# Performance work log

Measured on AMD Instinct MI355X. Metric: run time of the kernel, lower is better.

The kernel has to match this reference:

```python
import jax, jax.numpy as jnp
import numpy as np

NUM_HEADS = 32
NUM_KV_HEADS = 8  # num_heads // 4 (GQA)
HEAD_DIM = 64     # hidden_size // num_heads
ROPE_BASE = 10000.0


def _rotate_half(x):
    x1, x2 = jnp.split(x, 2, axis=-1)
    return jnp.concatenate((-x2, x1), axis=-1)


def _rope_cos_sin(seq_len, dtype):
    inv_freq = 1.0 / (ROPE_BASE ** (jnp.arange(0, HEAD_DIM, 2, dtype=jnp.float32) / HEAD_DIM))
    t = jnp.arange(seq_len, dtype=jnp.float32)
    freqs = jnp.outer(t, inv_freq)                 # [S, HEAD_DIM//2]
    emb = jnp.concatenate((freqs, freqs), axis=-1) # [S, HEAD_DIM]
    return jnp.cos(emb).astype(dtype), jnp.sin(emb).astype(dtype)


def setup_inputs() -> dict:
    key = jax.random.key(0)
    ks = jax.random.split(key, 5)
    B, S, H = 1, 2048, 2048
    KV = NUM_KV_HEADS * HEAD_DIM  # 512
    s = 0.02
    return {
        "hidden_states": jax.random.normal(ks[0], (B, S, H), jnp.float32),
        "Wq": jax.random.normal(ks[1], (H, H), jnp.float32) * s,
        "Wk": jax.random.normal(ks[2], (KV, H), jnp.float32) * s,
        "Wv": jax.random.normal(ks[3], (KV, H), jnp.float32) * s,
        "Wo": jax.random.normal(ks[4], (H, H), jnp.float32) * s,
    }


def reference(hidden_states, Wq, Wk, Wv, Wo):
    B, S, H = hidden_states.shape
    dtype = hidden_states.dtype
    # QKV projections (nn.Linear with weight [out,in], no bias)
    q = jnp.einsum("bsh,oh->bso", hidden_states, Wq)
    k = jnp.einsum("bsh,oh->bso", hidden_states, Wk)
    v = jnp.einsum("bsh,oh->bso", hidden_states, Wv)
    q = q.reshape(B, S, NUM_HEADS, HEAD_DIM).transpose(0, 2, 1, 3)      # [B,H,S,D]
    k = k.reshape(B, S, NUM_KV_HEADS, HEAD_DIM).transpose(0, 2, 1, 3)   # [B,KV,S,D]
    v = v.reshape(B, S, NUM_KV_HEADS, HEAD_DIM).transpose(0, 2, 1, 3)
    # RoPE
    cos, sin = _rope_cos_sin(S, dtype)  # [S,D] broadcast over batch/heads
    q = q * cos + _rotate_half(q) * sin
    k = k * cos + _rotate_half(k) * sin
    # GQA: repeat_interleave KV heads
    groups = NUM_HEADS // NUM_KV_HEADS
    k = jnp.repeat(k, groups, axis=1)
    v = jnp.repeat(v, groups, axis=1)
    # Attention: scores in fp32 softmax, causal mask (additive)
    scale = 1.0 / np.sqrt(HEAD_DIM)
    scores = jnp.einsum("bhqd,bhkd->bhqk", q, k) * scale
    causal = jnp.tril(jnp.ones((S, S), dtype=bool))
    scores = jnp.where(causal, scores, jnp.finfo(jnp.float32).min)
    probs = jax.nn.softmax(scores.astype(jnp.float32), axis=-1).astype(dtype)
    attn = jnp.einsum("bhqk,bhkd->bhqd", probs, v)
    attn = attn.transpose(0, 2, 1, 3).reshape(B, S, H)
    return jnp.einsum("bsh,oh->bso", attn, Wo)
```

## Files before the change

kernel.cpp:

```cpp
#include <hip/hip_runtime.h>
#include <hip/hip_bf16.h>
#include <math.h>

typedef __hip_bfloat16 bf16;
typedef __attribute__((ext_vector_type(8))) short short8;
typedef __attribute__((ext_vector_type(4))) short short4v;
typedef __attribute__((ext_vector_type(4))) float floatx4;

#define MFMA16(a, b, c) __builtin_amdgcn_mfma_f32_16x16x32_bf16((a), (b), (c), 0, 0, 0)

typedef const __attribute__((address_space(1))) void* as1_cvp;
typedef __attribute__((address_space(3))) void* as3_vp;

__device__ __forceinline__ void gload_lds16(const bf16* g, bf16* lds_uni) {
    __builtin_amdgcn_global_load_lds((as1_cvp)g, (as3_vp)lds_uni, 16, 0, 0);
}

__global__ __launch_bounds__(256) void cvt_all(
    const float* __restrict__ a0, const float* __restrict__ a1,
    const float* __restrict__ a2, const float* __restrict__ a3,
    const float* __restrict__ a4,
    bf16* __restrict__ d0, bf16* __restrict__ d1, bf16* __restrict__ d2,
    bf16* __restrict__ d3, bf16* __restrict__ d4)
{
    const int b = blockIdx.x;
    const float* src; bf16* dst; int off;
    if (b < 2048)      { src = a0; dst = d0; off = b; }
    else if (b < 4096) { src = a1; dst = d1; off = b - 2048; }
    else if (b < 4608) { src = a2; dst = d2; off = b - 4096; }
    else if (b < 5120) { src = a3; dst = d3; off = b - 4608; }
    else               { src = a4; dst = d4; off = b - 5120; }
    const int i = (off * 256 + threadIdx.x) * 8;
    const float4 x = *(const float4*)(src + i);
    const float4 y = *(const float4*)(src + i + 4);
    bf16 t[8];
    t[0] = __float2bfloat16(x.x); t[1] = __float2bfloat16(x.y);
    t[2] = __float2bfloat16(x.z); t[3] = __float2bfloat16(x.w);
    t[4] = __float2bfloat16(y.x); t[5] = __float2bfloat16(y.y);
    t[6] = __float2bfloat16(y.z); t[7] = __float2bfloat16(y.w);
    *(short8*)(dst + i) = *(const short8*)t;
}

__global__ __launch_bounds__(256) void gemm_qkv(
    const bf16* __restrict__ A, const bf16* __restrict__ Wq,
    const bf16* __restrict__ Wk, const bf16* __restrict__ Wv,
    bf16* __restrict__ qb, bf16* __restrict__ kb, bf16* __restrict__ vt)
{
    constexpr int K = 2048;
    __shared__ bf16 As[128 * 32];
    __shared__ bf16 Bs[128 * 32];

    const int tid  = threadIdx.x;
    const int lane = tid & 63;
    const int w    = tid >> 6;
    const int wm   = w >> 1, wn = w & 1;
    const int quad = lane >> 4, l15 = lane & 15;
    const int bx = blockIdx.x, by = blockIdx.y;

    const bf16* Bp; int bxl, mode;
    if (bx < 16)      { Bp = Wq; bxl = bx;      mode = 0; }
    else if (bx < 20) { Bp = Wk; bxl = bx - 16; mode = 1; }
    else              { Bp = Wv; bxl = bx - 20; mode = 2; }

    floatx4 acc[4][4];
#pragma unroll
    for (int i = 0; i < 4; ++i)
#pragma unroll
        for (int j = 0; j < 4; ++j) {
            floatx4 z = {0.f, 0.f, 0.f, 0.f};
            acc[i][j] = z;
        }

    const int srow = tid >> 2;
    const int sch  = (tid & 3) * 8;
    const bf16* gA = A  + (size_t)(by * 128 + srow) * K + sch;
    const bf16* gB = Bp + (size_t)(bxl * 128 + srow) * K + sch;
    const size_t K64 = (size_t)64 * K;
    bf16* ldsA0 = As + w * 512;
    bf16* ldsA1 = As + 2048 + w * 512;
    bf16* ldsB0 = Bs + w * 512;
    bf16* ldsB1 = Bs + 2048 + w * 512;

    for (int k0 = 0; k0 < K; k0 += 32) {
        gload_lds16(gA + k0,        ldsA0);
        gload_lds16(gA + K64 + k0,  ldsA1);
        gload_lds16(gB + k0,        ldsB0);
        gload_lds16(gB + K64 + k0,  ldsB1);
        __syncthreads();

        short8 af[4], bfrag[4];
#pragma unroll
        for (int i = 0; i < 4; ++i)
            af[i] = *(const short8*)&As[(wm * 64 + i * 16 + l15) * 32 + quad * 8];
#pragma unroll
        for (int j = 0; j < 4; ++j)
            bfrag[j] = *(const short8*)&Bs[(wn * 64 + j * 16 + l15) * 32 + quad * 8];
#pragma unroll
        for (int i = 0; i < 4; ++i)
#pragma unroll
            for (int j = 0; j < 4; ++j)
                acc[i][j] = MFMA16(af[i], bfrag[j], acc[i][j]);
        __syncthreads();
    }

    if (mode == 2) {
#pragma unroll
        for (int i = 0; i < 4; ++i)
#pragma unroll
            for (int j = 0; j < 4; ++j) {
                const int col = bxl * 128 + wn * 64 + j * 16 + l15;
                const int rowb = by * 128 + wm * 64 + i * 16 + quad * 4;
                bf16 t[4];
#pragma unroll
                for (int r = 0; r < 4; ++r) t[r] = __float2bfloat16(acc[i][j][r]);
                *(short4v*)&vt[(size_t)col * 2048 + rowb] = *(const short4v*)t;
            }
    } else {
        const int Nn = (mode == 0) ? 2048 : 512;
        bf16* C = (mode == 0) ? qb : kb;
        const float scale = (mode == 0) ? 0.125f : 1.0f;
        const float LOG2_1E4 = 13.28771237954945f;
        const float ifr0 = exp2f(-((float)l15) * (LOG2_1E4 / 32.f));
        const float ifr1 = exp2f(-((float)(16 + l15)) * (LOG2_1E4 / 32.f));
#pragma unroll
        for (int i = 0; i < 4; ++i) {
#pragma unroll
            for (int r = 0; r < 4; ++r) {
                const int row = by * 128 + wm * 64 + i * 16 + quad * 4 + r;
                float s0, c0, s1, c1;
                sincosf((float)row * ifr0, &s0, &c0);
                sincosf((float)row * ifr1, &s1, &c1);
#pragma unroll
                for (int j = 0; j < 4; ++j) {
                    const float x  = acc[i][j][r];
                    const float xp = acc[i][j ^ 2][r];
                    const float cs = (j & 1) ? c1 : c0;
                    const float sn = (j & 1) ? s1 : s0;
                    const float oo = (x * cs + ((j < 2) ? -xp : xp) * sn) * scale;
                    const int col = bxl * 128 + wn * 64 + j * 16 + l15;
                    C[(size_t)row * Nn + col] = __float2bfloat16(oo);
                }
            }
        }
    }
}

__global__ __launch_bounds__(256) void gemm_out(
    const bf16* __restrict__ A, const bf16* __restrict__ B, float* __restrict__ C,
    int N, int K)
{
    __shared__ bf16 As[128 * 32];
    __shared__ bf16 Bs[128 * 32];

    const int tid  = threadIdx.x;
    const int lane = tid & 63;
    const int w    = tid >> 6;
    const int wm   = w >> 1, wn = w & 1;
    const int quad = lane >> 4, l15 = lane & 15;
    const int bx = blockIdx.x, by = blockIdx.y;

    floatx4 acc[4][4];
#pragma unroll
    for (int i = 0; i < 4; ++i)
#pragma unroll
        for (int j = 0; j < 4; ++j) {
            floatx4 z = {0.f, 0.f, 0.f, 0.f};
            acc[i][j] = z;
        }

    const int srow = tid >> 2;
    const int sch  = (tid & 3) * 8;
    const bf16* gA = A + (size_t)(by * 128 + srow) * K + sch;
    const bf16* gB = B + (size_t)(bx * 128 + srow) * K + sch;
    const size_t K64 = (size_t)64 * K;
    bf16* ldsA0 = As + w * 512;
    bf16* ldsA1 = As + 2048 + w * 512;
    bf16* ldsB0 = Bs + w * 512;
    bf16* ldsB1 = Bs + 2048 + w * 512;

    for (int k0 = 0; k0 < K; k0 += 32) {
        gload_lds16(gA + k0,        ldsA0);
        gload_lds16(gA + K64 + k0,  ldsA1);
        gload_lds16(gB + k0,        ldsB0);
        gload_lds16(gB + K64 + k0,  ldsB1);
        __syncthreads();

        short8 af[4], bfrag[4];
#pragma unroll
        for (int i = 0; i < 4; ++i)
            af[i] = *(const short8*)&As[(wm * 64 + i * 16 + l15) * 32 + quad * 8];
#pragma unroll
        for (int j = 0; j < 4; ++j)
            bfrag[j] = *(const short8*)&Bs[(wn * 64 + j * 16 + l15) * 32 + quad * 8];
#pragma unroll
        for (int i = 0; i < 4; ++i)
#pragma unroll
            for (int j = 0; j < 4; ++j)
                acc[i][j] = MFMA16(af[i], bfrag[j], acc[i][j]);
        __syncthreads();
    }

#pragma unroll
    for (int i = 0; i < 4; ++i)
#pragma unroll
        for (int j = 0; j < 4; ++j)
#pragma unroll
            for (int r = 0; r < 4; ++r) {
                const int row = by * 128 + wm * 64 + i * 16 + quad * 4 + r;
                const int col = bx * 128 + wn * 64 + j * 16 + l15;
                C[(size_t)row * N + col] = acc[i][j][r];
            }
}

__global__ __launch_bounds__(256) void fattn4(
    const bf16* __restrict__ q, const bf16* __restrict__ k,
    const bf16* __restrict__ vt, bf16* __restrict__ o)
{
    __shared__ bf16 Ks[2][64 * 72];
    __shared__ bf16 Vs[2][64 * 72];
    __shared__ bf16 Ps[4][16 * 68];

    const int tpair = blockIdx.x;
    const int h = blockIdx.y;
    const int kvh = h >> 2;
    const int tid = threadIdx.x, lane = tid & 63, w = tid >> 6;
    const int quad = lane >> 4, l15 = lane & 15;
    bf16* P = Ps[w];

    short ob[8];
#pragma unroll
    for (int e = 0; e < 8; ++e) ob[e] = (short)0x3F80;
    const short8 ones = *(const short8*)ob;

    const int srow = tid >> 3;
    const int ch8  = (tid & 7) * 8;
    const bf16* kg = k  + (size_t)kvh * 64 + ch8;
    const bf16* vg = vt + (size_t)(kvh * 64 + srow) * 2048 + ch8;

#pragma unroll 1
    for (int ph = 0; ph < 2; ++ph) {
        const int a = ph ? (31 - tpair) : tpair;
        const int qrow0 = a * 64 + w * 16;

        short8 qf[2];
#pragma unroll
        for (int ks = 0; ks < 2; ++ks)
            qf[ks] = *(const short8*)&q[(size_t)(qrow0 + l15) * 2048 + h * 64 + ks * 32 + quad * 8];

        floatx4 o_acc[4], l_acc;
#pragma unroll
        for (int n4 = 0; n4 < 4; ++n4) {
            floatx4 z = {0.f, 0.f, 0.f, 0.f};
            o_acc[n4] = z;
        }
        { floatx4 z = {0.f, 0.f, 0.f, 0.f}; l_acc = z; }

        {
            short8 k0 = *(const short8*)(kg + (size_t)srow * 512);
            short8 k1 = *(const short8*)(kg + (size_t)(srow + 32) * 512);
            short8 v0 = *(const short8*)(vg);
            short8 v1 = *(const short8*)(vg + (size_t)32 * 2048);
            *(short8*)&Ks[0][srow * 72 + ch8]        = k0;
            *(short8*)&Ks[0][(srow + 32) * 72 + ch8] = k1;
            *(short8*)&Vs[0][srow * 72 + ch8]        = v0;
            *(short8*)&Vs[0][(srow + 32) * 72 + ch8] = v1;
        }
        __syncthreads();

        for (int kt = 0; kt <= a; ++kt) {
            const int buf = kt & 1;

            short8 nk0, nk1, nv0, nv1;
            if (kt < a) {
                const size_t kr = (size_t)((kt + 1) * 64) * 512;
                nk0 = *(const short8*)(kg + kr + (size_t)srow * 512);
                nk1 = *(const short8*)(kg + kr + (size_t)(srow + 32) * 512);
                nv0 = *(const short8*)(vg + (kt + 1) * 64);
                nv1 = *(const short8*)(vg + (size_t)32 * 2048 + (kt + 1) * 64);
            }

            floatx4 s_acc[4];
#pragma unroll
            for (int n = 0; n < 4; ++n) {
                floatx4 z = {0.f, 0.f, 0.f, 0.f};
                s_acc[n] = z;
            }
#pragma unroll
            for (int n = 0; n < 4; ++n)
#pragma unroll
                for (int ks = 0; ks < 2; ++ks) {
                    const short8 kf = *(const short8*)&Ks[buf][(n * 16 + l15) * 72 + ks * 32 + quad * 8];
                    s_acc[n] = MFMA16(qf[ks], kf, s_acc[n]);
                }

            if (kt < a) {
#pragma unroll
                for (int n = 0; n < 4; ++n)
#pragma unroll
                    for (int r = 0; r < 4; ++r)
                        P[(quad * 4 + r) * 68 + n * 16 + l15] = __float2bfloat16(__expf(s_acc[n][r]));
            } else {
#pragma unroll
                for (int n = 0; n < 4; ++n)
#pragma unroll
                    for (int r = 0; r < 4; ++r) {
                        const bool ok = (n * 16 + l15) <= (w * 16 + quad * 4 + r);
                        const float p = ok ? __expf(s_acc[n][r]) : 0.f;
                        P[(quad * 4 + r) * 68 + n * 16 + l15] = __float2bfloat16(p);
                    }
            }

#pragma unroll
            for (int ks2 = 0; ks2 < 2; ++ks2) {
                const short8 pf = *(const short8*)&P[l15 * 68 + ks2 * 32 + quad * 8];
                l_acc = MFMA16(pf, ones, l_acc);
#pragma unroll
                for (int n4 = 0; n4 < 4; ++n4) {
                    const short8 vf = *(const short8*)&Vs[buf][(n4 * 16 + l15) * 72 + ks2 * 32 + quad * 8];
                    o_acc[n4] = MFMA16(pf, vf, o_acc[n4]);
                }
            }

            if (kt < a) {
                *(short8*)&Ks[buf ^ 1][srow * 72 + ch8]        = nk0;
                *(short8*)&Ks[buf ^ 1][(srow + 32) * 72 + ch8] = nk1;
                *(short8*)&Vs[buf ^ 1][srow * 72 + ch8]        = nv0;
                *(short8*)&Vs[buf ^ 1][(srow + 32) * 72 + ch8] = nv1;
            }
            __syncthreads();
        }

#pragma unroll
        for (int n4 = 0; n4 < 4; ++n4)
#pragma unroll
            for (int r = 0; r < 4; ++r) {
                const float val = o_acc[n4][r] / l_acc[r];
                const int row = qrow0 + quad * 4 + r;
                const int col = h * 64 + n4 * 16 + l15;
                o[(size_t)row * 2048 + col] = __float2bfloat16(val);
            }
    }
}

extern "C" void kernel_launch(void* const* d_in, const int* in_sizes, int n_in,
                              void* d_out, int out_size, void* d_ws, size_t ws_size,
                              hipStream_t stream)
{
    const float* hs = (const float*)d_in[0];
    const float* Wq = (const float*)d_in[1];
    const float* Wk = (const float*)d_in[2];
    const float* Wv = (const float*)d_in[3];
    const float* Wo = (const float*)d_in[4];
    float* out = (float*)d_out;

    bf16* ws  = (bf16*)d_ws;
    bf16* hsb = ws;
    bf16* Wqb = hsb + 4194304;
    bf16* Wkb = Wqb + 4194304;
    bf16* Wvb = Wkb + 1048576;
    bf16* Wob = Wvb + 1048576;
    bf16* qb  = Wob + 4194304;
    bf16* kb  = qb  + 4194304;
    bf16* vtb = kb  + 1048576;
    bf16* ab  = vtb + 1048576;

    dim3 blk(256);
    cvt_all<<<7168, blk, 0, stream>>>(hs, Wq, Wk, Wv, Wo, hsb, Wqb, Wkb, Wvb, Wob);
    gemm_qkv<<<dim3(24, 16), blk, 0, stream>>>(hsb, Wqb, Wkb, Wvb, qb, kb, vtb);
    fattn4<<<dim3(16, 32), blk, 0, stream>>>(qb, kb, vtb, ab);
    gemm_out<<<dim3(16, 16), blk, 0, stream>>>(ab, Wob, out, 2048, 2048);
}
```

Baseline: 248.9 us.

## Double GEMM K-step and use 128-row query tiles in flash attention

```diff
diff --git a/kernel.cpp b/kernel.cpp
--- a/kernel.cpp
+++ b/kernel.cpp
@@ -41,14 +41,43 @@
     *(short8*)(dst + i) = *(const short8*)t;
 }
 
+#define GEMM_K_LOOP(K)                                                          \
+    for (int k0 = 0; k0 < (K); k0 += 64) {                                      \
+        gload_lds16(gA + k0,            ldsA0);                                 \
+        gload_lds16(gA + K64 + k0,      ldsA1);                                 \
+        gload_lds16(gB + k0,            ldsB0);                                 \
+        gload_lds16(gB + K64 + k0,      ldsB1);                                 \
+        gload_lds16(gA + k0 + 32,       ldsA0 + 4096);                          \
+        gload_lds16(gA + K64 + k0 + 32, ldsA1 + 4096);                          \
+        gload_lds16(gB + k0 + 32,       ldsB0 + 4096);                          \
+        gload_lds16(gB + K64 + k0 + 32, ldsB1 + 4096);                          \
+        __syncthreads();                                                        \
+        _Pragma("unroll")                                                       \
+        for (int hh = 0; hh < 2; ++hh) {                                        \
+            short8 af[4], bfr[4];                                               \
+            _Pragma("unroll")                                                   \
+            for (int i = 0; i < 4; ++i)                                         \
+                af[i] = *(const short8*)&As[hh * 4096 + (wm * 64 + i * 16 + l15) * 32 + quad * 8]; \
+            _Pragma("unroll")                                                   \
+            for (int j = 0; j < 4; ++j)                                         \
+                bfr[j] = *(const short8*)&Bs[hh * 4096 + (wn * 64 + j * 16 + l15) * 32 + quad * 8]; \
+            _Pragma("unroll")                                                   \
+            for (int i = 0; i < 4; ++i)                                         \
+                _Pragma("unroll")                                               \
+                for (int j = 0; j < 4; ++j)                                     \
+                    acc[i][j] = MFMA16(af[i], bfr[j], acc[i][j]);               \
+        }                                                                       \
+        __syncthreads();                                                        \
+    }
+
 __global__ __launch_bounds__(256) void gemm_qkv(
     const bf16* __restrict__ A, const bf16* __restrict__ Wq,
     const bf16* __restrict__ Wk, const bf16* __restrict__ Wv,
     bf16* __restrict__ qb, bf16* __restrict__ kb, bf16* __restrict__ vt)
 {
     constexpr int K = 2048;
-    __shared__ bf16 As[128 * 32];
-    __shared__ bf16 Bs[128 * 32];
+    __shared__ bf16 As[2 * 128 * 32];
+    __shared__ bf16 Bs[2 * 128 * 32];
 
     const int tid  = threadIdx.x;
     const int lane = tid & 63;
@@ -81,27 +110,7 @@
     bf16* ldsB0 = Bs + w * 512;
     bf16* ldsB1 = Bs + 2048 + w * 512;
 
-    for (int k0 = 0; k0 < K; k0 += 32) {
-        gload_lds16(gA + k0,        ldsA0);
-        gload_lds16(gA + K64 + k0,  ldsA1);
-        gload_lds16(gB + k0,        ldsB0);
-        gload_lds16(gB + K64 + k0,  ldsB1);
-        __syncthreads();
-
-        short8 af[4], bfrag[4];
-#pragma unroll
-        for (int i = 0; i < 4; ++i)
-            af[i] = *(const short8*)&As[(wm * 64 + i * 16 + l15) * 32 + quad * 8];
-#pragma unroll
-        for (int j = 0; j < 4; ++j)
-            bfrag[j] = *(const short8*)&Bs[(wn * 64 + j * 16 + l15) * 32 + quad * 8];
-#pragma unroll
-        for (int i = 0; i < 4; ++i)
-#pragma unroll
-            for (int j = 0; j < 4; ++j)
-                acc[i][j] = MFMA16(af[i], bfrag[j], acc[i][j]);
-        __syncthreads();
-    }
+    GEMM_K_LOOP(K)
 
     if (mode == 2) {
 #pragma unroll
@@ -149,8 +158,8 @@
     const bf16* __restrict__ A, const bf16* __restrict__ B, float* __restrict__ C,
     int N, int K)
 {
-    __shared__ bf16 As[128 * 32];
-    __shared__ bf16 Bs[128 * 32];
+    __shared__ bf16 As[2 * 128 * 32];
+    __shared__ bf16 Bs[2 * 128 * 32];
 
     const int tid  = threadIdx.x;
     const int lane = tid & 63;
@@ -178,27 +187,7 @@
     bf16* ldsB0 = Bs + w * 512;
     bf16* ldsB1 = Bs + 2048 + w * 512;
 
-    for (int k0 = 0; k0 < K; k0 += 32) {
-        gload_lds16(gA + k0,        ldsA0);
-        gload_lds16(gA + K64 + k0,  ldsA1);
-        gload_lds16(gB + k0,        ldsB0);
-        gload_lds16(gB + K64 + k0,  ldsB1);
-        __syncthreads();
-
-        short8 af[4], bfrag[4];
-#pragma unroll
-        for (int i = 0; i < 4; ++i)
-            af[i] = *(const short8*)&As[(wm * 64 + i * 16 + l15) * 32 + quad * 8];
-#pragma unroll
-        for (int j = 0; j < 4; ++j)
-            bfrag[j] = *(const short8*)&Bs[(wn * 64 + j * 16 + l15) * 32 + quad * 8];
-#pragma unroll
-        for (int i = 0; i < 4; ++i)
-#pragma unroll
-            for (int j = 0; j < 4; ++j)
-                acc[i][j] = MFMA16(af[i], bfrag[j], acc[i][j]);
-        __syncthreads();
-    }
+    GEMM_K_LOOP(K)
 
 #pragma unroll
     for (int i = 0; i < 4; ++i)
@@ -212,15 +201,15 @@
             }
 }
 
-__global__ __launch_bounds__(256) void fattn4(
+__global__ __launch_bounds__(256) void fattn5(
     const bf16* __restrict__ q, const bf16* __restrict__ k,
     const bf16* __restrict__ vt, bf16* __restrict__ o)
 {
     __shared__ bf16 Ks[2][64 * 72];
     __shared__ bf16 Vs[2][64 * 72];
-    __shared__ bf16 Ps[4][16 * 68];
-
-    const int tpair = blockIdx.x;
+    __shared__ bf16 Ps[4][32 * 68];
+
+    const int tp = blockIdx.x;
     const int h = blockIdx.y;
     const int kvh = h >> 2;
     const int tid = threadIdx.x, lane = tid & 63, w = tid >> 6;
@@ -239,21 +228,29 @@
 
 #pragma unroll 1
     for (int ph = 0; ph < 2; ++ph) {
-        const int a = ph ? (31 - tpair) : tpair;
-        const int qrow0 = a * 64 + w * 16;
-
-        short8 qf[2];
-#pragma unroll
-        for (int ks = 0; ks < 2; ++ks)
-            qf[ks] = *(const short8*)&q[(size_t)(qrow0 + l15) * 2048 + h * 64 + ks * 32 + quad * 8];
-
-        floatx4 o_acc[4], l_acc;
-#pragma unroll
-        for (int n4 = 0; n4 < 4; ++n4) {
+        const int t = ph ? (15 - tp) : tp;
+        const int qrow0 = t * 128 + w * 32;
+        const int ktmax = 2 * t + 1;
+
+        short8 qf[2][2];
+#pragma unroll
+        for (int mt = 0; mt < 2; ++mt)
+#pragma unroll
+            for (int ks = 0; ks < 2; ++ks)
+                qf[mt][ks] = *(const short8*)&q[(size_t)(qrow0 + mt * 16 + l15) * 2048
+                                                + h * 64 + ks * 32 + quad * 8];
+
+        floatx4 o_acc[2][4], l_acc[2];
+#pragma unroll
+        for (int mt = 0; mt < 2; ++mt) {
+#pragma unroll
+            for (int n4 = 0; n4 < 4; ++n4) {
+                floatx4 z = {0.f, 0.f, 0.f, 0.f};
+                o_acc[mt][n4] = z;
+            }
             floatx4 z = {0.f, 0.f, 0.f, 0.f};
-            o_acc[n4] = z;
-        }
-        { floatx4 z = {0.f, 0.f, 0.f, 0.f}; l_acc = z; }
+            l_acc[mt] = z;
+        }
 
         {
             short8 k0 = *(const short8*)(kg + (size_t)srow * 512);
@@ -267,11 +264,11 @@
         }
         __syncthreads();
 
-        for (int kt = 0; kt <= a; ++kt) {
+        for (int kt = 0; kt <= ktmax; ++kt) {
             const int buf = kt & 1;
 
             short8 nk0, nk1, nv0, nv1;
-            if (kt < a) {
+            if (kt < ktmax) {
                 const size_t kr = (size_t)((kt + 1) * 64) * 512;
                 nk0 = *(const short8*)(kg + kr + (size_t)srow * 512);
                 nk1 = *(const short8*)(kg + kr + (size_t)(srow + 32) * 512);
@@ -279,49 +276,63 @@
                 nv1 = *(const short8*)(vg + (size_t)32 * 2048 + (kt + 1) * 64);
             }
 
-            floatx4 s_acc[4];
-#pragma unroll
-            for (int n = 0; n < 4; ++n) {
-                floatx4 z = {0.f, 0.f, 0.f, 0.f};
-                s_acc[n] = z;
-            }
+            floatx4 s_acc[2][4];
+#pragma unroll
+            for (int mt = 0; mt < 2; ++mt)
+#pragma unroll
+                for (int n = 0; n < 4; ++n) {
+                    floatx4 z = {0.f, 0.f, 0.f, 0.f};
+                    s_acc[mt][n] = z;
+                }
 #pragma unroll
             for (int n = 0; n < 4; ++n)
 #pragma unroll
                 for (int ks = 0; ks < 2; ++ks) {
                     const short8 kf = *(const short8*)&Ks[buf][(n * 16 + l15) * 72 + ks * 32 + quad * 8];
-                    s_acc[n] = MFMA16(qf[ks], kf, s_acc[n]);
-                }
-
-            if (kt < a) {
-#pragma unroll
-                for (int n = 0; n < 4; ++n)
-#pragma unroll
-                    for (int r = 0; r < 4; ++r)
-                        P[(quad * 4 + r) * 68 + n * 16 + l15] = __float2bfloat16(__expf(s_acc[n][r]));
+                    s_acc[0][n] = MFMA16(qf[0][ks], kf, s_acc[0][n]);
+                    s_acc[1][n] = MFMA16(qf[1][ks], kf, s_acc[1][n]);
+                }
+
+            if (kt < 2 * t) {
+#pragma unroll
+                for (int mt = 0; mt < 2; ++mt)
+#pragma unroll
+                    for (int n = 0; n < 4; ++n)
+#pragma unroll
+                        for (int r = 0; r < 4; ++r)
+                            P[(mt * 16 + quad * 4 + r) * 68 + n * 16 + l15] =
+                                __float2bfloat16(__expf(s_acc[mt][n][r]));
             } else {
-#pragma unroll
-                for (int n = 0; n < 4; ++n)
-#pragma unroll
-                    for (int r = 0; r < 4; ++r) {
-                        const bool ok = (n * 16 + l15) <= (w * 16 + quad * 4 + r);
-                        const float p = ok ? __expf(s_acc[n][r]) : 0.f;
-                        P[(quad * 4 + r) * 68 + n * 16 + l15] = __float2bfloat16(p);
-                    }
+                const int base = kt * 64 - t * 128;
+#pragma unroll
+                for (int mt = 0; mt < 2; ++mt)
+#pragma unroll
+                    for (int n = 0; n < 4; ++n)
+#pragma unroll
+                        for (int r = 0; r < 4; ++r) {
+                            const bool okc = (base + n * 16 + l15) <= (w * 32 + mt * 16 + quad * 4 + r);
+                            const float p = okc ? __expf(s_acc[mt][n][r]) : 0.f;
+                            P[(mt * 16 + quad * 4 + r) * 68 + n * 16 + l15] = __float2bfloat16(p);
+                        }
             }
 
 #pragma unroll
             for (int ks2 = 0; ks2 < 2; ++ks2) {
-                const short8 pf = *(const short8*)&P[l15 * 68 + ks2 * 32 + quad * 8];
-                l_acc = MFMA16(pf, ones, l_acc);
+                short8 pf[2];
+#pragma unroll
+                for (int mt = 0; mt < 2; ++mt) {
+                    pf[mt] = *(const short8*)&P[(mt * 16 + l15) * 68 + ks2 * 32 + quad * 8];
+                    l_acc[mt] = MFMA16(pf[mt], ones, l_acc[mt]);
+                }
 #pragma unroll
                 for (int n4 = 0; n4 < 4; ++n4) {
                     const short8 vf = *(const short8*)&Vs[buf][(n4 * 16 + l15) * 72 + ks2 * 32 + quad * 8];
-                    o_acc[n4] = MFMA16(pf, vf, o_acc[n4]);
-                }
-            }
-
-            if (kt < a) {
+                    o_acc[0][n4] = MFMA16(pf[0], vf, o_acc[0][n4]);
+                    o_acc[1][n4] = MFMA16(pf[1], vf, o_acc[1][n4]);
+                }
+            }
+
+            if (kt < ktmax) {
                 *(short8*)&Ks[buf ^ 1][srow * 72 + ch8]        = nk0;
                 *(short8*)&Ks[buf ^ 1][(srow + 32) * 72 + ch8] = nk1;
                 *(short8*)&Vs[buf ^ 1][srow * 72 + ch8]        = nv0;
@@ -331,14 +342,16 @@
         }
 
 #pragma unroll
-        for (int n4 = 0; n4 < 4; ++n4)
-#pragma unroll
-            for (int r = 0; r < 4; ++r) {
-                const float val = o_acc[n4][r] / l_acc[r];
-                const int row = qrow0 + quad * 4 + r;
-                const int col = h * 64 + n4 * 16 + l15;
-                o[(size_t)row * 2048 + col] = __float2bfloat16(val);
-            }
+        for (int mt = 0; mt < 2; ++mt)
+#pragma unroll
+            for (int n4 = 0; n4 < 4; ++n4)
+#pragma unroll
+                for (int r = 0; r < 4; ++r) {
+                    const float val = o_acc[mt][n4][r] / l_acc[mt][r];
+                    const int row = qrow0 + mt * 16 + quad * 4 + r;
+                    const int col = h * 64 + n4 * 16 + l15;
+                    o[(size_t)row * 2048 + col] = __float2bfloat16(val);
+                }
     }
 }
 
@@ -367,6 +380,6 @@
     dim3 blk(256);
     cvt_all<<<7168, blk, 0, stream>>>(hs, Wq, Wk, Wv, Wo, hsb, Wqb, Wkb, Wvb, Wob);
     gemm_qkv<<<dim3(24, 16), blk, 0, stream>>>(hsb, Wqb, Wkb, Wvb, qb, kb, vtb);
-    fattn4<<<dim3(16, 32), blk, 0, stream>>>(qb, kb, vtb, ab);
+    fattn5<<<dim3(8, 32), blk, 0, stream>>>(qb, kb, vtb, ab);
     gemm_out<<<dim3(16, 16), blk, 0, stream>>>(ab, Wob, out, 2048, 2048);
 }
```

Measured after the change: 247.6 us. Within noise of the previous version (-0.5%).

## Split-K the Q and output projections and add merge kernels with RoPE

Applied to the files above, without the earlier changes.

```diff
diff --git a/kernel.cpp b/kernel.cpp
--- a/kernel.cpp
+++ b/kernel.cpp
@@ -41,14 +41,44 @@
     *(short8*)(dst + i) = *(const short8*)t;
 }
 
+#define GEMM_K_LOOP(KB, LDK)                                                    \
+    for (int k0 = 0; k0 < (KB); k0 += 64) {                                     \
+        gload_lds16(gA + k0,            ldsA0);                                 \
+        gload_lds16(gA + K64 + k0,      ldsA1);                                 \
+        gload_lds16(gB + k0,            ldsB0);                                 \
+        gload_lds16(gB + K64 + k0,      ldsB1);                                 \
+        gload_lds16(gA + k0 + 32,       ldsA0 + 4096);                          \
+        gload_lds16(gA + K64 + k0 + 32, ldsA1 + 4096);                          \
+        gload_lds16(gB + k0 + 32,       ldsB0 + 4096);                          \
+        gload_lds16(gB + K64 + k0 + 32, ldsB1 + 4096);                          \
+        __syncthreads();                                                        \
+        _Pragma("unroll")                                                       \
+        for (int hh = 0; hh < 2; ++hh) {                                        \
+            short8 af[4], bfr[4];                                               \
+            _Pragma("unroll")                                                   \
+            for (int i = 0; i < 4; ++i)                                         \
+                af[i] = *(const short8*)&As[hh * 4096 + (wm * 64 + i * 16 + l15) * 32 + quad * 8]; \
+            _Pragma("unroll")                                                   \
+            for (int j = 0; j < 4; ++j)                                         \
+                bfr[j] = *(const short8*)&Bs[hh * 4096 + (wn * 64 + j * 16 + l15) * 32 + quad * 8]; \
+            _Pragma("unroll")                                                   \
+            for (int i = 0; i < 4; ++i)                                         \
+                _Pragma("unroll")                                               \
+                for (int j = 0; j < 4; ++j)                                     \
+                    acc[i][j] = MFMA16(af[i], bfr[j], acc[i][j]);               \
+        }                                                                       \
+        __syncthreads();                                                        \
+    }
+
 __global__ __launch_bounds__(256) void gemm_qkv(
     const bf16* __restrict__ A, const bf16* __restrict__ Wq,
     const bf16* __restrict__ Wk, const bf16* __restrict__ Wv,
-    bf16* __restrict__ qb, bf16* __restrict__ kb, bf16* __restrict__ vt)
-{
-    constexpr int K = 2048;
-    __shared__ bf16 As[128 * 32];
-    __shared__ bf16 Bs[128 * 32];
+    bf16* __restrict__ qp0, bf16* __restrict__ qp1,
+    bf16* __restrict__ kb, bf16* __restrict__ vt)
+{
+    constexpr int LDK = 2048;
+    __shared__ bf16 As[2 * 128 * 32];
+    __shared__ bf16 Bs[2 * 128 * 32];
 
     const int tid  = threadIdx.x;
     const int lane = tid & 63;
@@ -57,10 +87,11 @@
     const int quad = lane >> 4, l15 = lane & 15;
     const int bx = blockIdx.x, by = blockIdx.y;
 
-    const bf16* Bp; int bxl, mode;
-    if (bx < 16)      { Bp = Wq; bxl = bx;      mode = 0; }
-    else if (bx < 20) { Bp = Wk; bxl = bx - 16; mode = 1; }
-    else              { Bp = Wv; bxl = bx - 20; mode = 2; }
+    const bf16* Bp; int bxl, mode, kbeg, kext;
+    if (bx < 4)       { Bp = Wk; bxl = bx;      mode = 1; kbeg = 0;    kext = 2048; }
+    else if (bx < 8)  { Bp = Wv; bxl = bx - 4;  mode = 2; kbeg = 0;    kext = 2048; }
+    else if (bx < 24) { Bp = Wq; bxl = bx - 8;  mode = 0; kbeg = 0;    kext = 1024; }
+    else              { Bp = Wq; bxl = bx - 24; mode = 3; kbeg = 1024; kext = 1024; }
 
     floatx4 acc[4][4];
 #pragma unroll
@@ -73,35 +104,15 @@
 
     const int srow = tid >> 2;
     const int sch  = (tid & 3) * 8;
-    const bf16* gA = A  + (size_t)(by * 128 + srow) * K + sch;
-    const bf16* gB = Bp + (size_t)(bxl * 128 + srow) * K + sch;
-    const size_t K64 = (size_t)64 * K;
+    const bf16* gA = A  + (size_t)(by * 128 + srow) * LDK + kbeg + sch;
+    const bf16* gB = Bp + (size_t)(bxl * 128 + srow) * LDK + kbeg + sch;
+    const size_t K64 = (size_t)64 * LDK;
     bf16* ldsA0 = As + w * 512;
     bf16* ldsA1 = As + 2048 + w * 512;
     bf16* ldsB0 = Bs + w * 512;
     bf16* ldsB1 = Bs + 2048 + w * 512;
 
-    for (int k0 = 0; k0 < K; k0 += 32) {
-        gload_lds16(gA + k0,        ldsA0);
-        gload_lds16(gA + K64 + k0,  ldsA1);
-        gload_lds16(gB + k0,        ldsB0);
-        gload_lds16(gB + K64 + k0,  ldsB1);
-        __syncthreads();
-
-        short8 af[4], bfrag[4];
-#pragma unroll
-        for (int i = 0; i < 4; ++i)
-            af[i] = *(const short8*)&As[(wm * 64 + i * 16 + l15) * 32 + quad * 8];
-#pragma unroll
-        for (int j = 0; j < 4; ++j)
-            bfrag[j] = *(const short8*)&Bs[(wn * 64 + j * 16 + l15) * 32 + quad * 8];
-#pragma unroll
-        for (int i = 0; i < 4; ++i)
-#pragma unroll
-            for (int j = 0; j < 4; ++j)
-                acc[i][j] = MFMA16(af[i], bfrag[j], acc[i][j]);
-        __syncthreads();
-    }
+    GEMM_K_LOOP(kext, LDK)
 
     if (mode == 2) {
 #pragma unroll
@@ -115,10 +126,7 @@
                 for (int r = 0; r < 4; ++r) t[r] = __float2bfloat16(acc[i][j][r]);
                 *(short4v*)&vt[(size_t)col * 2048 + rowb] = *(const short4v*)t;
             }
-    } else {
-        const int Nn = (mode == 0) ? 2048 : 512;
-        bf16* C = (mode == 0) ? qb : kb;
-        const float scale = (mode == 0) ? 0.125f : 1.0f;
+    } else if (mode == 1) {
         const float LOG2_1E4 = 13.28771237954945f;
         const float ifr0 = exp2f(-((float)l15) * (LOG2_1E4 / 32.f));
         const float ifr1 = exp2f(-((float)(16 + l15)) * (LOG2_1E4 / 32.f));
@@ -136,28 +144,79 @@
                     const float xp = acc[i][j ^ 2][r];
                     const float cs = (j & 1) ? c1 : c0;
                     const float sn = (j & 1) ? s1 : s0;
-                    const float oo = (x * cs + ((j < 2) ? -xp : xp) * sn) * scale;
+                    const float oo = x * cs + ((j < 2) ? -xp : xp) * sn;
                     const int col = bxl * 128 + wn * 64 + j * 16 + l15;
-                    C[(size_t)row * Nn + col] = __float2bfloat16(oo);
+                    kb[(size_t)row * 512 + col] = __float2bfloat16(oo);
                 }
             }
         }
+    } else {
+        bf16* C = (mode == 0) ? qp0 : qp1;
+#pragma unroll
+        for (int i = 0; i < 4; ++i)
+#pragma unroll
+            for (int j = 0; j < 4; ++j)
+#pragma unroll
+                for (int r = 0; r < 4; ++r) {
+                    const int row = by * 128 + wm * 64 + i * 16 + quad * 4 + r;
+                    const int col = bxl * 128 + wn * 64 + j * 16 + l15;
+                    C[(size_t)row * 2048 + col] = __float2bfloat16(acc[i][j][r]);
+                }
     }
 }
 
+__global__ __launch_bounds__(256) void merge_q(
+    const bf16* __restrict__ qp0, const bf16* __restrict__ qp1,
+    bf16* __restrict__ qb)
+{
+    const int t = threadIdx.x;
+    const int row = blockIdx.x * 2 + (t >> 7);
+    const int i7 = t & 127;
+    const int head = i7 >> 2;
+    const int dd0 = (i7 & 3) * 8;
+    const size_t base = (size_t)row * 2048 + head * 64;
+
+    short8 a0 = *(const short8*)(qp0 + base + dd0);
+    short8 a1 = *(const short8*)(qp1 + base + dd0);
+    short8 b0 = *(const short8*)(qp0 + base + 32 + dd0);
+    short8 b1 = *(const short8*)(qp1 + base + 32 + dd0);
+    const bf16* pa0 = (const bf16*)&a0; const bf16* pa1 = (const bf16*)&a1;
+    const bf16* pb0 = (const bf16*)&b0; const bf16* pb1 = (const bf16*)&b1;
+
+    const float LOG2_1E4 = 13.28771237954945f;
+    bf16 o0[8], o1[8];
+#pragma unroll
+    for (int j = 0; j < 8; ++j) {
+        const float x = __bfloat162float(pa0[j]) + __bfloat162float(pa1[j]);
+        const float y = __bfloat162float(pb0[j]) + __bfloat162float(pb1[j]);
+        const float ifr = exp2f(-((float)(dd0 + j)) * (LOG2_1E4 / 32.f));
+        float sn, cs;
+        sincosf((float)row * ifr, &sn, &cs);
+        o0[j] = __float2bfloat16((x * cs - y * sn) * 0.125f);
+        o1[j] = __float2bfloat16((y * cs + x * sn) * 0.125f);
+    }
+    *(short8*)(qb + base + dd0)      = *(const short8*)o0;
+    *(short8*)(qb + base + 32 + dd0) = *(const short8*)o1;
+}
+
 __global__ __launch_bounds__(256) void gemm_out(
-    const bf16* __restrict__ A, const bf16* __restrict__ B, float* __restrict__ C,
-    int N, int K)
-{
-    __shared__ bf16 As[128 * 32];
-    __shared__ bf16 Bs[128 * 32];
+    const bf16* __restrict__ A, const bf16* __restrict__ B,
+    float* __restrict__ op0, float* __restrict__ op1)
+{
+    constexpr int LDK = 2048;
+    __shared__ bf16 As[2 * 128 * 32];
+    __shared__ bf16 Bs[2 * 128 * 32];
 
     const int tid  = threadIdx.x;
     const int lane = tid & 63;
     const int w    = tid >> 6;
     const int wm   = w >> 1, wn = w & 1;
     const int quad = lane >> 4, l15 = lane & 15;
-    const int bx = blockIdx.x, by = blockIdx.y;
+    const int bxr = blockIdx.x, by = blockIdx.y;
+    const int kh  = bxr >> 4;
+    const int bx  = bxr & 15;
+    const int kbeg = kh * 1024;
+    float* C = kh ? op1 : op0;
 
     floatx4 acc[4][4];
 #pragma unroll
@@ -170,35 +229,15 @@
 
     const int srow = tid >> 2;
     const int sch  = (tid & 3) * 8;
-    const bf16* gA = A + (size_t)(by * 128 + srow) * K + sch;
-    const bf16* gB = B + (size_t)(bx * 128 + srow) * K + sch;
-    const size_t K64 = (size_t)64 * K;
+    const bf16* gA = A + (size_t)(by * 128 + srow) * LDK + kbeg + sch;
+    const bf16* gB = B + (size_t)(bx * 128 + srow) * LDK + kbeg + sch;
+    const size_t K64 = (size_t)64 * LDK;
     bf16* ldsA0 = As + w * 512;
     bf16* ldsA1 = As + 2048 + w * 512;
     bf16* ldsB0 = Bs + w * 512;
     bf16* ldsB1 = Bs + 2048 + w * 512;
 
-    for (int k0 = 0; k0 < K; k0 += 32) {
-        gload_lds16(gA + k0,        ldsA0);
-        gload_lds16(gA + K64 + k0,  ldsA1);
-        gload_lds16(gB + k0,        ldsB0);
-        gload_lds16(gB + K64 + k0,  ldsB1);
-        __syncthreads();
-
-        short8 af[4], bfrag[4];
-#pragma unroll
-        for (int i = 0; i < 4; ++i)
-            af[i] = *(const short8*)&As[(wm * 64 + i * 16 + l15) * 32 + quad * 8];
-#pragma unroll
-        for (int j = 0; j < 4; ++j)
-            bfrag[j] = *(const short8*)&Bs[(wn * 64 + j * 16 + l15) * 32 + quad * 8];
-#pragma unroll
-        for (int i = 0; i < 4; ++i)
-#pragma unroll
-            for (int j = 0; j < 4; ++j)
-                acc[i][j] = MFMA16(af[i], bfrag[j], acc[i][j]);
-        __syncthreads();
-    }
+    GEMM_K_LOOP(1024, LDK)
 
 #pragma unroll
     for (int i = 0; i < 4; ++i)
@@ -208,8 +247,23 @@
             for (int r = 0; r < 4; ++r) {
                 const int row = by * 128 + wm * 64 + i * 16 + quad * 4 + r;
                 const int col = bx * 128 + wn * 64 + j * 16 + l15;
-                C[(size_t)row * N + col] = acc[i][j][r];
-            }
+                C[(size_t)row * 2048 + col] = acc[i][j][r];
+            }
+}
+
+__global__ __launch_bounds__(256) void merge_out(
+    const float* __restrict__ op0, const float* __restrict__ op1,
+    float* __restrict__ out)
+{
+    const int i = (blockIdx.x * 256 + threadIdx.x) * 8;
+    const float4 a0 = *(const float4*)(op0 + i);
+    const float4 a1 = *(const float4*)(op0 + i + 4);
+    const float4 b0 = *(const float4*)(op1 + i);
+    const float4 b1 = *(const float4*)(op1 + i + 4);
+    float4 r0 = {a0.x + b0.x, a0.y + b0.y, a0.z + b0.z, a0.w + b0.w};
+    float4 r1 = {a1.x + b1.x, a1.y + b1.y, a1.z + b1.z, a1.w + b1.w};
+    *(float4*)(out + i)     = r0;
+    *(float4*)(out + i + 4) = r1;
 }
 
 __global__ __launch_bounds__(256) void fattn4(
@@ -304,8 +358,8 @@
                 for (int n = 0; n < 4; ++n)
 #pragma unroll
                     for (int r = 0; r < 4; ++r) {
-                        const bool ok = (n * 16 + l15) <= (w * 16 + quad * 4 + r);
-                        const float p = ok ? __expf(s_acc[n][r]) : 0.f;
+                        const bool okc = (n * 16 + l15) <= (w * 16 + quad * 4 + r);
+                        const float p = okc ? __expf(s_acc[n][r]) : 0.f;
                         P[(quad * 4 + r) * 68 + n * 16 + l15] = __float2bfloat16(p);
                     }
             }
@@ -355,18 +409,24 @@
 
     bf16* ws  = (bf16*)d_ws;
     bf16* hsb = ws;
-    bf16* Wqb = hsb + 4194304;
-    bf16* Wkb = Wqb + 4194304;
-    bf16* Wvb = Wkb + 1048576;
-    bf16* Wob = Wvb + 1048576;
-    bf16* qb  = Wob + 4194304;
-    bf16* kb  = qb  + 4194304;
-    bf16* vtb = kb  + 1048576;
-    bf16* ab  = vtb + 1048576;
+    bf16* Wqb = ws + 4194304;
+    bf16* Wkb = ws + 8388608;
+    bf16* Wvb = ws + 9437184;
+    bf16* qb  = ws + 10485760;
+    bf16* kb  = ws + 14680064;
+    bf16* vtb = ws + 15728640;
+    bf16* ab  = ws + 16777216;
+    bf16* Wob = ws + 20971520;
+    bf16* qp0 = ws + 25165824;
+    bf16* qp1 = ws + 29360128;
+    float* op0 = (float*)d_ws;
+    float* op1 = (float*)d_ws + 4194304;
 
     dim3 blk(256);
     cvt_all<<<7168, blk, 0, stream>>>(hs, Wq, Wk, Wv, Wo, hsb, Wqb, Wkb, Wvb, Wob);
-    gemm_qkv<<<dim3(24, 16), blk, 0, stream>>>(hsb, Wqb, Wkb, Wvb, qb, kb, vtb);
+    gemm_qkv<<<dim3(40, 16), blk, 0, stream>>>(hsb, Wqb, Wkb, Wvb, qp0, qp1, kb, vtb);
+    merge_q<<<1024, blk, 0, stream>>>(qp0, qp1, qb);
     fattn4<<<dim3(16, 32), blk, 0, stream>>>(qb, kb, vtb, ab);
-    gemm_out<<<dim3(16, 16), blk, 0, stream>>>(ab, Wob, out, 2048, 2048);
-}
+    gemm_out<<<dim3(32, 16), blk, 0, stream>>>(ab, Wob, op0, op1);
+    merge_out<<<2048, blk, 0, stream>>>(op0, op1, out);
+}
```

After: 254.1 us. +2.1%, slower.
